# Optimization experiments

Hardware: AMD Instinct MI355X
Metric: run time of the kernel (lower is better)

Reference implementation:

```python
import jax, jax.numpy as jnp
import numpy as np

D_MODEL = 1024
NUM_HEADS = 16
HEAD_DIM = D_MODEL // NUM_HEADS


def setup_inputs() -> dict:
    key = jax.random.key(0)
    ks = jax.random.split(key, 11)
    B, S = 4, 2048
    scale = 1.0 / np.sqrt(D_MODEL)
    inp = {
        'q': jax.random.normal(ks[0], (B, S, D_MODEL), jnp.float32),
        'k': jax.random.normal(ks[1], (B, S, D_MODEL), jnp.float32),
        'v': jax.random.normal(ks[2], (B, S, D_MODEL), jnp.float32),
        'Wq': jax.random.normal(ks[3], (D_MODEL, D_MODEL), jnp.float32) * scale,
        'bq': jnp.zeros((D_MODEL,), jnp.float32),
        'Wk': jax.random.normal(ks[4], (D_MODEL, D_MODEL), jnp.float32) * scale,
        'bk': jnp.zeros((D_MODEL,), jnp.float32),
        'Wv': jax.random.normal(ks[5], (D_MODEL, D_MODEL), jnp.float32) * scale,
        'bv': jnp.zeros((D_MODEL,), jnp.float32),
        'Wo': jax.random.normal(ks[6], (D_MODEL, D_MODEL), jnp.float32) * scale,
        'bo': jnp.zeros((D_MODEL,), jnp.float32),
    }
    return inp


def _split_heads(x):
    B, S, _ = x.shape
    return x.reshape(B, S, NUM_HEADS, HEAD_DIM).transpose(0, 2, 1, 3)  # [B,H,S,Dh]


def reference(q, k, v, Wq, bq, Wk, bk, Wv, bv, Wo, bo):
    Q = _split_heads(q @ Wq.T + bq)
    K = _split_heads(k @ Wk.T + bk)
    V = _split_heads(v @ Wv.T + bv)
    scores = jnp.einsum('bhqd,bhkd->bhqk', Q, K) / jnp.sqrt(jnp.float32(HEAD_DIM))
    attn = jax.nn.softmax(scores, axis=-1)
    out = jnp.einsum('bhqk,bhkd->bhqd', attn, V)  # [B,H,S,Dh]
    B, _, S, _ = out.shape
    out = out.transpose(0, 2, 1, 3).reshape(B, S, D_MODEL)
    return out @ Wo.T + bo
```

## Files before the change

### kernel.cpp

```cpp
#include <hip/hip_runtime.h>
#include <hip/hip_bf16.h>

#define DMODEL 1024
#define NHEADS 16
#define HDIM 64

typedef __bf16 bf16_t;
typedef __bf16 bf16x8 __attribute__((ext_vector_type(8)));
typedef float  f32x4  __attribute__((ext_vector_type(4)));
typedef float  f32x16 __attribute__((ext_vector_type(16)));

__device__ __forceinline__ bf16_t f2bf(float f) {
    unsigned int u = __builtin_bit_cast(unsigned int, f);
    u += 0x7FFF + ((u >> 16) & 1);
    unsigned short h = (unsigned short)(u >> 16);
    return __builtin_bit_cast(bf16_t, h);
}

__device__ __forceinline__ unsigned cvt_pk_bf16(float lo, float hi) {
    unsigned r;
    asm("v_cvt_pk_bf16_f32 %0, %1, %2" : "=v"(r) : "v"(lo), "v"(hi));
    return r;
}

__device__ __forceinline__ void gld_lds16(const bf16_t* g, bf16_t* l) {
    __builtin_amdgcn_global_load_lds(
        (const __attribute__((address_space(1))) unsigned int*)g,
        (__attribute__((address_space(3))) unsigned int*)l, 16, 0, 0);
}

__global__ __launch_bounds__(256) void cast_all(const float* __restrict__ Wq,
                                                const float* __restrict__ Wk,
                                                const float* __restrict__ Wv,
                                                const float* __restrict__ Wo,
                                                const float* __restrict__ q,
                                                const float* __restrict__ k,
                                                const float* __restrict__ v,
                                                bf16_t* __restrict__ Wall,
                                                bf16_t* __restrict__ qb,
                                                bf16_t* __restrict__ kb,
                                                bf16_t* __restrict__ vb,
                                                int nw, int na) {
    const int y = blockIdx.y;
    const float* s;
    bf16_t* d;
    int n;
    if (y == 0)      { s = Wq; d = Wall;               n = nw; }
    else if (y == 1) { s = Wk; d = Wall + (size_t)nw;  n = nw; }
    else if (y == 2) { s = Wv; d = Wall + 2 * (size_t)nw; n = nw; }
    else if (y == 3) { s = Wo; d = Wall + 3 * (size_t)nw; n = nw; }
    else if (y == 4) { s = q;  d = qb; n = na; }
    else if (y == 5) { s = k;  d = kb; n = na; }
    else             { s = v;  d = vb; n = na; }
    int i = blockIdx.x * blockDim.x + threadIdx.x;
    int stride = gridDim.x * blockDim.x;
    for (int idx = i * 4; idx < n; idx += stride * 4) {
        float4 vv = *reinterpret_cast<const float4*>(s + idx);
        uint2 u;
        u.x = cvt_pk_bf16(vv.x, vv.y);
        u.y = cvt_pk_bf16(vv.z, vv.w);
        *reinterpret_cast<uint2*>(d + idx) = u;
    }
}

__global__ __launch_bounds__(256) void gemm_qkv(const bf16_t* __restrict__ qb,
                                                const bf16_t* __restrict__ kb,
                                                const bf16_t* __restrict__ vb,
                                                const bf16_t* __restrict__ Wall,
                                                const float* __restrict__ bq,
                                                const float* __restrict__ bk,
                                                const float* __restrict__ bv,
                                                bf16_t* __restrict__ Qp,
                                                bf16_t* __restrict__ Kp,
                                                bf16_t* __restrict__ VtG,
                                                int M, float qscale, int S) {
    __shared__ bf16_t Asmem[2][128 * 32];
    __shared__ bf16_t Bsmem[2][128 * 32];
    const int K = DMODEL, N = DMODEL;
    const int z = blockIdx.z;
    const bf16_t* Ab = (z == 0) ? qb : (z == 1) ? kb : vb;
    const bf16_t* W = Wall + (size_t)z * DMODEL * DMODEL;
    const float* bias = (z == 0) ? bq : (z == 1) ? bk : bv;
    const float scale = (z == 0) ? qscale : 1.0f;

    const int m0 = blockIdx.x * 128;
    const int n0 = blockIdx.y * 128;
    const int tid = threadIdx.x;
    const int wave = tid >> 6, lane = tid & 63;
    const int wm = wave >> 1, wn = wave & 1;
    const int lr = lane & 15, lg = lane >> 4;
    const int srow = lane >> 2, scol = (lane & 3) * 8;

    f32x4 acc[4][4];
#pragma unroll
    for (int mi = 0; mi < 4; ++mi)
#pragma unroll
        for (int ni = 0; ni < 4; ++ni) acc[mi][ni] = (f32x4){0.f, 0.f, 0.f, 0.f};

#pragma unroll
    for (int i = 0; i < 2; ++i) {
        int c = wave * 2 + i;
        gld_lds16(Ab + (size_t)(m0 + c * 16 + srow) * K + scol, &Asmem[0][c * 512]);
        gld_lds16(W + (size_t)(n0 + c * 16 + srow) * K + scol, &Bsmem[0][c * 512]);
    }
    asm volatile("s_waitcnt vmcnt(0)" ::: "memory");
    __syncthreads();

    const int nk = K / 32;
    for (int t = 0; t < nk; ++t) {
        const int cur = t & 1, nxt = cur ^ 1;
        const int ktn = (t + 1) * 32;
        if (t + 1 < nk) {
#pragma unroll
            for (int i = 0; i < 2; ++i) {
                int c = wave * 2 + i;
                gld_lds16(Ab + (size_t)(m0 + c * 16 + srow) * K + ktn + scol, &Asmem[nxt][c * 512]);
                gld_lds16(W + (size_t)(n0 + c * 16 + srow) * K + ktn + scol, &Bsmem[nxt][c * 512]);
            }
        }
        bf16x8 af[4], bfr[4];
#pragma unroll
        for (int mi = 0; mi < 4; ++mi)
            af[mi] = *reinterpret_cast<const bf16x8*>(&Asmem[cur][(wm * 64 + mi * 16 + lr) * 32 + lg * 8]);
#pragma unroll
        for (int ni = 0; ni < 4; ++ni)
            bfr[ni] = *reinterpret_cast<const bf16x8*>(&Bsmem[cur][(wn * 64 + ni * 16 + lr) * 32 + lg * 8]);
#pragma unroll
        for (int mi = 0; mi < 4; ++mi)
#pragma unroll
            for (int ni = 0; ni < 4; ++ni)
                acc[mi][ni] = __builtin_amdgcn_mfma_f32_16x16x32_bf16(af[mi], bfr[ni], acc[mi][ni], 0, 0, 0);
        asm volatile("s_waitcnt vmcnt(0)" ::: "memory");
        __syncthreads();
    }

#pragma unroll
    for (int mi = 0; mi < 4; ++mi) {
        int row = m0 + wm * 64 + mi * 16 + lg * 4;
#pragma unroll
        for (int ni = 0; ni < 4; ++ni) {
            int col = n0 + wn * 64 + ni * 16 + lr;
            float bv_ = bias[col];
            if (z == 2) {
                union { bf16_t b[4]; uint2 u; } pq;
#pragma unroll
                for (int r = 0; r < 4; ++r) pq.b[r] = f2bf(acc[mi][ni][r] + bv_);
                int b_ = row / S, s_ = row % S;
                size_t addr = (((size_t)b_ * NHEADS + (col >> 6)) * HDIM + (col & 63)) * (size_t)S + s_;
                *reinterpret_cast<uint2*>(VtG + addr) = pq.u;
            } else {
                bf16_t* Cb = (z == 0) ? Qp : Kp;
#pragma unroll
                for (int r = 0; r < 4; ++r)
                    Cb[(size_t)(row + r) * N + col] = f2bf((acc[mi][ni][r] + bv_) * scale);
            }
        }
    }
}

__global__ __launch_bounds__(256) void gemm_out(const bf16_t* __restrict__ Ab,
                                                const bf16_t* __restrict__ W,
                                                const float* __restrict__ bias,
                                                float* __restrict__ Cout,
                                                int M, int N, int K) {
    __shared__ bf16_t Asmem[2][128 * 32];
    __shared__ bf16_t Bsmem[2][128 * 32];
    const int m0 = blockIdx.x * 128;
    const int n0 = blockIdx.y * 128;
    const int tid = threadIdx.x;
    const int wave = tid >> 6, lane = tid & 63;
    const int wm = wave >> 1, wn = wave & 1;
    const int lr = lane & 15, lg = lane >> 4;
    const int srow = lane >> 2, scol = (lane & 3) * 8;

    f32x4 acc[4][4];
#pragma unroll
    for (int mi = 0; mi < 4; ++mi)
#pragma unroll
        for (int ni = 0; ni < 4; ++ni) acc[mi][ni] = (f32x4){0.f, 0.f, 0.f, 0.f};

#pragma unroll
    for (int i = 0; i < 2; ++i) {
        int c = wave * 2 + i;
        gld_lds16(Ab + (size_t)(m0 + c * 16 + srow) * K + scol, &Asmem[0][c * 512]);
        gld_lds16(W + (size_t)(n0 + c * 16 + srow) * K + scol, &Bsmem[0][c * 512]);
    }
    asm volatile("s_waitcnt vmcnt(0)" ::: "memory");
    __syncthreads();

    const int nk = K / 32;
    for (int t = 0; t < nk; ++t) {
        const int cur = t & 1, nxt = cur ^ 1;
        const int ktn = (t + 1) * 32;
        if (t + 1 < nk) {
#pragma unroll
            for (int i = 0; i < 2; ++i) {
                int c = wave * 2 + i;
                gld_lds16(Ab + (size_t)(m0 + c * 16 + srow) * K + ktn + scol, &Asmem[nxt][c * 512]);
                gld_lds16(W + (size_t)(n0 + c * 16 + srow) * K + ktn + scol, &Bsmem[nxt][c * 512]);
            }
        }
        bf16x8 af[4], bfr[4];
#pragma unroll
        for (int mi = 0; mi < 4; ++mi)
            af[mi] = *reinterpret_cast<const bf16x8*>(&Asmem[cur][(wm * 64 + mi * 16 + lr) * 32 + lg * 8]);
#pragma unroll
        for (int ni = 0; ni < 4; ++ni)
            bfr[ni] = *reinterpret_cast<const bf16x8*>(&Bsmem[cur][(wn * 64 + ni * 16 + lr) * 32 + lg * 8]);
#pragma unroll
        for (int mi = 0; mi < 4; ++mi)
#pragma unroll
            for (int ni = 0; ni < 4; ++ni)
                acc[mi][ni] = __builtin_amdgcn_mfma_f32_16x16x32_bf16(af[mi], bfr[ni], acc[mi][ni], 0, 0, 0);
        asm volatile("s_waitcnt vmcnt(0)" ::: "memory");
        __syncthreads();
    }

#pragma unroll
    for (int mi = 0; mi < 4; ++mi) {
        int row = m0 + wm * 64 + mi * 16 + lg * 4;
#pragma unroll
        for (int ni = 0; ni < 4; ++ni) {
            int col = n0 + wn * 64 + ni * 16 + lr;
            float bv = bias[col];
#pragma unroll
            for (int r = 0; r < 4; ++r)
                Cout[(size_t)(row + r) * N + col] = acc[mi][ni][r] + bv;
        }
    }
}

__global__ __launch_bounds__(256, 4) void attn_kernel(const bf16_t* __restrict__ Qp,
                                                      const bf16_t* __restrict__ Kp,
                                                      const bf16_t* __restrict__ VtG,
                                                      bf16_t* __restrict__ AO, int S) {
    __shared__ bf16_t KsA[64 * 64], KsB[64 * 64];
    __shared__ bf16_t VtA[64 * 64], VtB[64 * 64];
    const int tid = threadIdx.x;
    const int wave = tid >> 6, lane = tid & 63;
    const int ql = lane & 31;
    const int hi = lane >> 5;
    const int bh = blockIdx.x;
    const int b = bh >> 4, h = bh & 15;
    const int qt = blockIdx.y;
    const size_t base = ((size_t)b * S) * DMODEL + (size_t)h * HDIM;
    const size_t vbase = (size_t)bh * HDIM * (size_t)S;

    const int qrow = qt * 128 + wave * 32 + ql;
    bf16x8 qf[4];
#pragma unroll
    for (int kc = 0; kc < 4; ++kc)
        qf[kc] = *reinterpret_cast<const bf16x8*>(Qp + base + (size_t)qrow * DMODEL + kc * 16 + hi * 8);

    f32x16 o0{}, o1{};
    float l_r = 0.f;

    const int r0 = tid >> 3;
    const int swz = ((tid & 7) ^ (r0 & 7)) * 8;
    const bf16_t* Kb = Kp + base;
    const bf16_t* Vb = VtG + vbase;

    auto stageK = [&](int kv, bf16_t* buf) {
        gld_lds16(Kb + (size_t)(kv + r0) * DMODEL + swz, buf + wave * 512);
        gld_lds16(Kb + (size_t)(kv + r0 + 32) * DMODEL + swz, buf + 2048 + wave * 512);
    };
    auto stageV = [&](int kv, bf16_t* buf) {
        gld_lds16(Vb + (size_t)r0 * S + kv + swz, buf + wave * 512);
        gld_lds16(Vb + (size_t)(r0 + 32) * S + kv + swz, buf + 2048 + wave * 512);
    };

    const int NT = S / 64;
    auto tile = [&](const bf16_t* Kc, const bf16_t* Vc, bf16_t* Kn, bf16_t* Vn, int t) {
        if (t + 1 < NT) {
            stageK((t + 1) * 64, Kn);
            stageV((t + 1) * 64, Vn);
        }

        f32x16 s0{}, s1{};
        __builtin_amdgcn_s_setprio(1);
#pragma unroll
        for (int kc = 0; kc < 4; ++kc) {
            bf16x8 kf = *reinterpret_cast<const bf16x8*>(
                &Kc[ql * 64 + (((2 * kc + hi) ^ (ql & 7)) * 8)]);
            s0 = __builtin_amdgcn_mfma_f32_32x32x16_bf16(kf, qf[kc], s0, 0, 0, 0);
        }
#pragma unroll
        for (int kc = 0; kc < 4; ++kc) {
            bf16x8 kf = *reinterpret_cast<const bf16x8*>(
                &Kc[(32 + ql) * 64 + (((2 * kc + hi) ^ (ql & 7)) * 8)]);
            s1 = __builtin_amdgcn_mfma_f32_32x32x16_bf16(kf, qf[kc], s1, 0, 0, 0);
        }
        __builtin_amdgcn_s_setprio(0);

        float p0[16], p1[16];
#pragma unroll
        for (int r = 0; r < 16; ++r) {
            p0[r] = __builtin_amdgcn_exp2f(s0[r]);
            p1[r] = __builtin_amdgcn_exp2f(s1[r]);
        }
        float a4[8];
#pragma unroll
        for (int j = 0; j < 8; ++j)
            a4[j] = (p0[2 * j] + p0[2 * j + 1]) + (p1[2 * j] + p1[2 * j + 1]);
        float a2[4];
#pragma unroll
        for (int j = 0; j < 4; ++j) a2[j] = a4[2 * j] + a4[2 * j + 1];
        l_r += (a2[0] + a2[1]) + (a2[2] + a2[3]);

        unsigned w[8][2];
#pragma unroll
        for (int j = 0; j < 4; ++j) {
            w[j][0] = cvt_pk_bf16(p0[4 * j], p0[4 * j + 1]);
            w[j][1] = cvt_pk_bf16(p0[4 * j + 2], p0[4 * j + 3]);
            w[4 + j][0] = cvt_pk_bf16(p1[4 * j], p1[4 * j + 1]);
            w[4 + j][1] = cvt_pk_bf16(p1[4 * j + 2], p1[4 * j + 3]);
        }

#pragma unroll
        for (int kq = 0; kq < 4; ++kq) {
            unsigned own0 = hi ? w[2 * kq + 1][0] : w[2 * kq][0];
            unsigned own1 = hi ? w[2 * kq + 1][1] : w[2 * kq][1];
            unsigned y0 = hi ? w[2 * kq][0] : w[2 * kq + 1][0];
            unsigned y1 = hi ? w[2 * kq][1] : w[2 * kq + 1][1];
            y0 = (unsigned)__shfl_xor((int)y0, 32, 64);
            y1 = (unsigned)__shfl_xor((int)y1, 32, 64);
            union { unsigned u[4]; bf16x8 v; } pb;
            pb.u[0] = hi ? y0 : own0;
            pb.u[1] = hi ? y1 : own1;
            pb.u[2] = hi ? own0 : y0;
            pb.u[3] = hi ? own1 : y1;
            bf16x8 vf0 = *reinterpret_cast<const bf16x8*>(
                &Vc[ql * 64 + (((2 * kq + hi) ^ (ql & 7)) * 8)]);
            bf16x8 vf1 = *reinterpret_cast<const bf16x8*>(
                &Vc[(32 + ql) * 64 + (((2 * kq + hi) ^ (ql & 7)) * 8)]);
            __builtin_amdgcn_s_setprio(1);
            o0 = __builtin_amdgcn_mfma_f32_32x32x16_bf16(vf0, pb.v, o0, 0, 0, 0);
            o1 = __builtin_amdgcn_mfma_f32_32x32x16_bf16(vf1, pb.v, o1, 0, 0, 0);
            __builtin_amdgcn_s_setprio(0);
        }

        asm volatile("s_waitcnt vmcnt(0)" ::: "memory");
        __syncthreads();
    };

    stageK(0, KsA);
    stageV(0, VtA);
    asm volatile("s_waitcnt vmcnt(0)" ::: "memory");
    __syncthreads();

    for (int t = 0; t < NT; t += 2) {
        tile(KsA, VtA, KsB, VtB, t);
        tile(KsB, VtB, KsA, VtA, t + 1);
    }

    float l_all = l_r + __shfl_xor(l_r, 32, 64);
    float inv = 1.f / l_all;
    bf16_t* Ao = AO + base + (size_t)qrow * DMODEL;
#pragma unroll
    for (int j = 0; j < 4; ++j) {
        uint2 u0, u1;
        u0.x = cvt_pk_bf16(o0[4 * j] * inv, o0[4 * j + 1] * inv);
        u0.y = cvt_pk_bf16(o0[4 * j + 2] * inv, o0[4 * j + 3] * inv);
        *reinterpret_cast<uint2*>(Ao + 8 * j + 4 * hi) = u0;
        u1.x = cvt_pk_bf16(o1[4 * j] * inv, o1[4 * j + 1] * inv);
        u1.y = cvt_pk_bf16(o1[4 * j + 2] * inv, o1[4 * j + 3] * inv);
        *reinterpret_cast<uint2*>(Ao + 32 + 8 * j + 4 * hi) = u1;
    }
}

extern "C" void kernel_launch(void* const* d_in, const int* in_sizes, int n_in,
                              void* d_out, int out_size, void* d_ws, size_t ws_size,
                              hipStream_t stream) {
    const float* q  = (const float*)d_in[0];
    const float* k  = (const float*)d_in[1];
    const float* v  = (const float*)d_in[2];
    const float* Wq = (const float*)d_in[3];
    const float* bq = (const float*)d_in[4];
    const float* Wk = (const float*)d_in[5];
    const float* bk = (const float*)d_in[6];
    const float* Wv = (const float*)d_in[7];
    const float* bv = (const float*)d_in[8];
    const float* Wo = (const float*)d_in[9];
    const float* bo = (const float*)d_in[10];

    const int M = in_sizes[0] / DMODEL;
    const int S = 2048;
    const int B = M / S;

    bf16_t* ws  = (bf16_t*)d_ws;
    const size_t WSZ = (size_t)DMODEL * DMODEL;
    const size_t MSZ = (size_t)M * DMODEL;
    bf16_t* Wqb = ws;
    bf16_t* Wob = Wqb + 3 * WSZ;
    bf16_t* Qp  = Wob + WSZ;
    bf16_t* Kp  = Qp + MSZ;
    bf16_t* VtG = Kp + MSZ;
    bf16_t* shX = VtG + MSZ;
    bf16_t* qb  = (bf16_t*)d_out;
    bf16_t* kb  = qb + MSZ;
    bf16_t* vb  = shX;
    bf16_t* AO  = shX;

    cast_all<<<dim3(2048, 7), 256, 0, stream>>>(Wq, Wk, Wv, Wo, q, k, v,
                                                ws, qb, kb, vb,
                                                DMODEL * DMODEL, M * DMODEL);

    const float qscale = 0.125f * 1.44269504088896f;
    gemm_qkv<<<dim3(M / 128, DMODEL / 128, 3), 256, 0, stream>>>(
        qb, kb, vb, Wqb, bq, bk, bv, Qp, Kp, VtG, M, qscale, S);

    attn_kernel<<<dim3(B * NHEADS, S / 128), 256, 0, stream>>>(Qp, Kp, VtG, AO, S);

    gemm_out<<<dim3(M / 128, DMODEL / 128), 256, 0, stream>>>(
        AO, Wob, bo, (float*)d_out, M, DMODEL, DMODEL);
}
```

Baseline: 231.7 us.

## Write K/V in MFMA fragment order and load directly from global in attention

The QKV GEMM epilogue now writes K and V in a pre-swizzled per-lane fragment layout, transposing the K MFMA operands so each lane holds four contiguous head-dim values. The attention kernel drops its LDS double buffering and barriers and instead has every wave load its K/V fragments straight from global memory with coalesced 16-byte loads per tile. This removes LDS staging and syncs, but each of the four waves in a block now reads the same K/V tile separately through the cache, and the loads are no longer prefetched a tile ahead. Launch bounds are relaxed to 2 blocks per CU to leave room for the extra fragment registers.

```diff
diff --git a/kernel.cpp b/kernel.cpp
--- a/kernel.cpp
+++ b/kernel.cpp
@@ -71,8 +71,8 @@
                                                 const float* __restrict__ bk,
                                                 const float* __restrict__ bv,
                                                 bf16_t* __restrict__ Qp,
-                                                bf16_t* __restrict__ Kp,
-                                                bf16_t* __restrict__ VtG,
+                                                bf16_t* __restrict__ Kf,
+                                                bf16_t* __restrict__ Vf,
                                                 int M, float qscale, int S) {
     __shared__ bf16_t Asmem[2][128 * 32];
     __shared__ bf16_t Bsmem[2][128 * 32];
@@ -81,7 +81,6 @@
     const bf16_t* Ab = (z == 0) ? qb : (z == 1) ? kb : vb;
     const bf16_t* W = Wall + (size_t)z * DMODEL * DMODEL;
     const float* bias = (z == 0) ? bq : (z == 1) ? bk : bv;
-    const float scale = (z == 0) ? qscale : 1.0f;
 
     const int m0 = blockIdx.x * 128;
     const int n0 = blockIdx.y * 128;
@@ -125,34 +124,64 @@
 #pragma unroll
         for (int ni = 0; ni < 4; ++ni)
             bfr[ni] = *reinterpret_cast<const bf16x8*>(&Bsmem[cur][(wn * 64 + ni * 16 + lr) * 32 + lg * 8]);
-#pragma unroll
-        for (int mi = 0; mi < 4; ++mi)
-#pragma unroll
-            for (int ni = 0; ni < 4; ++ni)
-                acc[mi][ni] = __builtin_amdgcn_mfma_f32_16x16x32_bf16(af[mi], bfr[ni], acc[mi][ni], 0, 0, 0);
+        if (z == 1) {
+#pragma unroll
+            for (int mi = 0; mi < 4; ++mi)
+#pragma unroll
+                for (int ni = 0; ni < 4; ++ni)
+                    acc[mi][ni] = __builtin_amdgcn_mfma_f32_16x16x32_bf16(bfr[ni], af[mi], acc[mi][ni], 0, 0, 0);
+        } else {
+#pragma unroll
+            for (int mi = 0; mi < 4; ++mi)
+#pragma unroll
+                for (int ni = 0; ni < 4; ++ni)
+                    acc[mi][ni] = __builtin_amdgcn_mfma_f32_16x16x32_bf16(af[mi], bfr[ni], acc[mi][ni], 0, 0, 0);
+        }
         asm volatile("s_waitcnt vmcnt(0)" ::: "memory");
         __syncthreads();
     }
 
 #pragma unroll
     for (int mi = 0; mi < 4; ++mi) {
-        int row = m0 + wm * 64 + mi * 16 + lg * 4;
 #pragma unroll
         for (int ni = 0; ni < 4; ++ni) {
-            int col = n0 + wn * 64 + ni * 16 + lr;
-            float bv_ = bias[col];
-            if (z == 2) {
-                union { bf16_t b[4]; uint2 u; } pq;
-#pragma unroll
-                for (int r = 0; r < 4; ++r) pq.b[r] = f2bf(acc[mi][ni][r] + bv_);
-                int b_ = row / S, s_ = row % S;
-                size_t addr = (((size_t)b_ * NHEADS + (col >> 6)) * HDIM + (col & 63)) * (size_t)S + s_;
-                *reinterpret_cast<uint2*>(VtG + addr) = pq.u;
+            if (z == 0) {
+                int row = m0 + wm * 64 + mi * 16 + lg * 4;
+                int col = n0 + wn * 64 + ni * 16 + lr;
+                float bv_ = bias[col];
+#pragma unroll
+                for (int r = 0; r < 4; ++r)
+                    Qp[(size_t)(row + r) * N + col] = f2bf((acc[mi][ni][r] + bv_) * qscale);
+            } else if (z == 1) {
+                int s_abs = m0 + wm * 64 + mi * 16 + lr;
+                int d_abs = n0 + wn * 64 + ni * 16 + lg * 4;
+                float4 bv4 = *reinterpret_cast<const float4*>(bias + d_abs);
+                int b_ = s_abs / S, s = s_abs % S;
+                int h = d_abs >> 6, d = d_abs & 63;
+                int kc = d >> 4, hia = (d >> 3) & 1, e0 = d & 7;
+                size_t off = (size_t)(b_ * NHEADS + h) * ((size_t)S * HDIM)
+                           + (size_t)((((s >> 6) * 2 + ((s >> 5) & 1)) * 4 + kc) * 512
+                                      + ((s & 31) + 32 * hia) * 8 + e0);
+                uint2 u;
+                u.x = cvt_pk_bf16(acc[mi][ni][0] + bv4.x, acc[mi][ni][1] + bv4.y);
+                u.y = cvt_pk_bf16(acc[mi][ni][2] + bv4.z, acc[mi][ni][3] + bv4.w);
+                *reinterpret_cast<uint2*>(Kf + off) = u;
             } else {
-                bf16_t* Cb = (z == 0) ? Qp : Kp;
-#pragma unroll
-                for (int r = 0; r < 4; ++r)
-                    Cb[(size_t)(row + r) * N + col] = f2bf((acc[mi][ni][r] + bv_) * scale);
+                int row = m0 + wm * 64 + mi * 16 + lg * 4;
+                int col = n0 + wn * 64 + ni * 16 + lr;
+                float bv_ = bias[col];
+                int b_ = row / S, s0 = row % S;
+                int h = col >> 6, d = col & 63;
+                int t_ = s0 >> 6, klk = s0 & 63;
+                int kq = klk >> 4, hia = (klk >> 3) & 1, e0 = klk & 7;
+                int gd = d >> 5;
+                size_t off = (size_t)(b_ * NHEADS + h) * ((size_t)S * HDIM)
+                           + (size_t)(((t_ * 2 + gd) * 4 + kq) * 512
+                                      + ((d & 31) + 32 * hia) * 8 + e0);
+                uint2 u;
+                u.x = cvt_pk_bf16(acc[mi][ni][0] + bv_, acc[mi][ni][1] + bv_);
+                u.y = cvt_pk_bf16(acc[mi][ni][2] + bv_, acc[mi][ni][3] + bv_);
+                *reinterpret_cast<uint2*>(Vf + off) = u;
             }
         }
     }
@@ -230,12 +259,10 @@
     }
 }
 
-__global__ __launch_bounds__(256, 4) void attn_kernel(const bf16_t* __restrict__ Qp,
-                                                      const bf16_t* __restrict__ Kp,
-                                                      const bf16_t* __restrict__ VtG,
+__global__ __launch_bounds__(256, 2) void attn_kernel(const bf16_t* __restrict__ Qp,
+                                                      const bf16_t* __restrict__ KfG,
+                                                      const bf16_t* __restrict__ VfG,
                                                       bf16_t* __restrict__ AO, int S) {
-    __shared__ bf16_t KsA[64 * 64], KsB[64 * 64];
-    __shared__ bf16_t VtA[64 * 64], VtB[64 * 64];
     const int tid = threadIdx.x;
     const int wave = tid >> 6, lane = tid & 63;
     const int ql = lane & 31;
@@ -244,7 +271,7 @@
     const int b = bh >> 4, h = bh & 15;
     const int qt = blockIdx.y;
     const size_t base = ((size_t)b * S) * DMODEL + (size_t)h * HDIM;
-    const size_t vbase = (size_t)bh * HDIM * (size_t)S;
+    const size_t fbase = (size_t)bh * ((size_t)S * HDIM);
 
     const int qrow = qt * 128 + wave * 32 + ql;
     bf16x8 qf[4];
@@ -255,53 +282,42 @@
     f32x16 o0{}, o1{};
     float l_r = 0.f;
 
-    const int r0 = tid >> 3;
-    const int swz = ((tid & 7) ^ (r0 & 7)) * 8;
-    const bf16_t* Kb = Kp + base;
-    const bf16_t* Vb = VtG + vbase;
-
-    auto stageK = [&](int kv, bf16_t* buf) {
-        gld_lds16(Kb + (size_t)(kv + r0) * DMODEL + swz, buf + wave * 512);
-        gld_lds16(Kb + (size_t)(kv + r0 + 32) * DMODEL + swz, buf + 2048 + wave * 512);
-    };
-    auto stageV = [&](int kv, bf16_t* buf) {
-        gld_lds16(Vb + (size_t)r0 * S + kv + swz, buf + wave * 512);
-        gld_lds16(Vb + (size_t)(r0 + 32) * S + kv + swz, buf + 2048 + wave * 512);
-    };
+    const bf16_t* Kf = KfG + fbase;
+    const bf16_t* Vf = VfG + fbase;
+    const int le = lane * 8;
 
     const int NT = S / 64;
-    auto tile = [&](const bf16_t* Kc, const bf16_t* Vc, bf16_t* Kn, bf16_t* Vn, int t) {
-        if (t + 1 < NT) {
-            stageK((t + 1) * 64, Kn);
-            stageV((t + 1) * 64, Vn);
+    for (int t = 0; t < NT; ++t) {
+        const bf16_t* kt = Kf + t * 4096;
+        const bf16_t* vt = Vf + t * 4096;
+        bf16x8 kf0[4], kf1[4], vf0[4], vf1[4];
+#pragma unroll
+        for (int c = 0; c < 4; ++c) {
+            kf0[c] = *reinterpret_cast<const bf16x8*>(kt + c * 512 + le);
+            kf1[c] = *reinterpret_cast<const bf16x8*>(kt + 2048 + c * 512 + le);
+            vf0[c] = *reinterpret_cast<const bf16x8*>(vt + c * 512 + le);
+            vf1[c] = *reinterpret_cast<const bf16x8*>(vt + 2048 + c * 512 + le);
         }
 
         f32x16 s0{}, s1{};
         __builtin_amdgcn_s_setprio(1);
 #pragma unroll
-        for (int kc = 0; kc < 4; ++kc) {
-            bf16x8 kf = *reinterpret_cast<const bf16x8*>(
-                &Kc[ql * 64 + (((2 * kc + hi) ^ (ql & 7)) * 8)]);
-            s0 = __builtin_amdgcn_mfma_f32_32x32x16_bf16(kf, qf[kc], s0, 0, 0, 0);
-        }
-#pragma unroll
-        for (int kc = 0; kc < 4; ++kc) {
-            bf16x8 kf = *reinterpret_cast<const bf16x8*>(
-                &Kc[(32 + ql) * 64 + (((2 * kc + hi) ^ (ql & 7)) * 8)]);
-            s1 = __builtin_amdgcn_mfma_f32_32x32x16_bf16(kf, qf[kc], s1, 0, 0, 0);
-        }
+        for (int kc = 0; kc < 4; ++kc)
+            s0 = __builtin_amdgcn_mfma_f32_32x32x16_bf16(kf0[kc], qf[kc], s0, 0, 0, 0);
+#pragma unroll
+        for (int kc = 0; kc < 4; ++kc)
+            s1 = __builtin_amdgcn_mfma_f32_32x32x16_bf16(kf1[kc], qf[kc], s1, 0, 0, 0);
         __builtin_amdgcn_s_setprio(0);
 
-        float p0[16], p1[16];
 #pragma unroll
         for (int r = 0; r < 16; ++r) {
-            p0[r] = __builtin_amdgcn_exp2f(s0[r]);
-            p1[r] = __builtin_amdgcn_exp2f(s1[r]);
+            s0[r] = __builtin_amdgcn_exp2f(s0[r]);
+            s1[r] = __builtin_amdgcn_exp2f(s1[r]);
         }
         float a4[8];
 #pragma unroll
         for (int j = 0; j < 8; ++j)
-            a4[j] = (p0[2 * j] + p0[2 * j + 1]) + (p1[2 * j] + p1[2 * j + 1]);
+            a4[j] = (s0[2 * j] + s0[2 * j + 1]) + (s1[2 * j] + s1[2 * j + 1]);
         float a2[4];
 #pragma unroll
         for (int j = 0; j < 4; ++j) a2[j] = a4[2 * j] + a4[2 * j + 1];
@@ -310,10 +326,10 @@
         unsigned w[8][2];
 #pragma unroll
         for (int j = 0; j < 4; ++j) {
-            w[j][0] = cvt_pk_bf16(p0[4 * j], p0[4 * j + 1]);
-            w[j][1] = cvt_pk_bf16(p0[4 * j + 2], p0[4 * j + 3]);
-            w[4 + j][0] = cvt_pk_bf16(p1[4 * j], p1[4 * j + 1]);
-            w[4 + j][1] = cvt_pk_bf16(p1[4 * j + 2], p1[4 * j + 3]);
+            w[j][0] = cvt_pk_bf16(s0[4 * j], s0[4 * j + 1]);
+            w[j][1] = cvt_pk_bf16(s0[4 * j + 2], s0[4 * j + 3]);
+            w[4 + j][0] = cvt_pk_bf16(s1[4 * j], s1[4 * j + 1]);
+            w[4 + j][1] = cvt_pk_bf16(s1[4 * j + 2], s1[4 * j + 3]);
         }
 
 #pragma unroll
@@ -329,28 +345,11 @@
             pb.u[1] = hi ? y1 : own1;
             pb.u[2] = hi ? own0 : y0;
             pb.u[3] = hi ? own1 : y1;
-            bf16x8 vf0 = *reinterpret_cast<const bf16x8*>(
-                &Vc[ql * 64 + (((2 * kq + hi) ^ (ql & 7)) * 8)]);
-            bf16x8 vf1 = *reinterpret_cast<const bf16x8*>(
-                &Vc[(32 + ql) * 64 + (((2 * kq + hi) ^ (ql & 7)) * 8)]);
             __builtin_amdgcn_s_setprio(1);
-            o0 = __builtin_amdgcn_mfma_f32_32x32x16_bf16(vf0, pb.v, o0, 0, 0, 0);
-            o1 = __builtin_amdgcn_mfma_f32_32x32x16_bf16(vf1, pb.v, o1, 0, 0, 0);
+            o0 = __builtin_amdgcn_mfma_f32_32x32x16_bf16(vf0[kq], pb.v, o0, 0, 0, 0);
+            o1 = __builtin_amdgcn_mfma_f32_32x32x16_bf16(vf1[kq], pb.v, o1, 0, 0, 0);
             __builtin_amdgcn_s_setprio(0);
         }
-
-        asm volatile("s_waitcnt vmcnt(0)" ::: "memory");
-        __syncthreads();
-    };
-
-    stageK(0, KsA);
-    stageV(0, VtA);
-    asm volatile("s_waitcnt vmcnt(0)" ::: "memory");
-    __syncthreads();
-
-    for (int t = 0; t < NT; t += 2) {
-        tile(KsA, VtA, KsB, VtB, t);
-        tile(KsB, VtB, KsA, VtA, t + 1);
     }
 
     float l_all = l_r + __shfl_xor(l_r, 32, 64);
@@ -393,9 +392,9 @@
     bf16_t* Wqb = ws;
     bf16_t* Wob = Wqb + 3 * WSZ;
     bf16_t* Qp  = Wob + WSZ;
-    bf16_t* Kp  = Qp + MSZ;
-    bf16_t* VtG = Kp + MSZ;
-    bf16_t* shX = VtG + MSZ;
+    bf16_t* Kf  = Qp + MSZ;
+    bf16_t* Vf  = Kf + MSZ;
+    bf16_t* shX = Vf + MSZ;
     bf16_t* qb  = (bf16_t*)d_out;
     bf16_t* kb  = qb + MSZ;
     bf16_t* vb  = shX;
@@ -407,9 +406,9 @@
 
     const float qscale = 0.125f * 1.44269504088896f;
     gemm_qkv<<<dim3(M / 128, DMODEL / 128, 3), 256, 0, stream>>>(
-        qb, kb, vb, Wqb, bq, bk, bv, Qp, Kp, VtG, M, qscale, S);
-
-    attn_kernel<<<dim3(B * NHEADS, S / 128), 256, 0, stream>>>(Qp, Kp, VtG, AO, S);
+        qb, kb, vb, Wqb, bq, bk, bv, Qp, Kf, Vf, M, qscale, S);
+
+    attn_kernel<<<dim3(B * NHEADS, S / 128), 256, 0, stream>>>(Qp, Kf, Vf, AO, S);
 
     gemm_out<<<dim3(M / 128, DMODEL / 128), 256, 0, stream>>>(
         AO, Wob, bo, (float*)d_out, M, DMODEL, DMODEL);
```

Result: slower. 244.3 us (+5.4%).
